# Kernel optimization log

Hardware: AMD Instinct MI355X
Metric: run time of the kernel (lower is better)

Reference implementation:

```python
import jax, jax.numpy as jnp
import numpy as np


def gcn_conv(x, edge_index, W, b):
    """PyG GCNConv with default add_self_loops=True, normalize=True.

    edge_index[0] = source (j), edge_index[1] = target (i), flow source_to_target.
    norm = deg^{-1/2}[j] * deg^{-1/2}[i], deg computed on target col with
    self-loops included (edge weight 1).
    """
    N = x.shape[0]
    loops = jnp.arange(N, dtype=edge_index.dtype)
    row = jnp.concatenate([edge_index[0], loops])  # sources j
    col = jnp.concatenate([edge_index[1], loops])  # targets i

    ones = jnp.ones(row.shape[0], dtype=x.dtype)
    deg = jax.ops.segment_sum(ones, col, num_segments=N)  # [N]
    deg_inv_sqrt = jnp.where(deg > 0, jax.lax.rsqrt(deg), 0.0)
    norm = deg_inv_sqrt[row] * deg_inv_sqrt[col]  # [E+N]

    h = x @ W  # [N, out] linear transform before propagation
    msg = norm[:, None] * h[row]  # gather from sources
    out = jax.ops.segment_sum(msg, col, num_segments=N)  # scatter-add to targets
    return out + b


def setup_inputs() -> dict:
    key = jax.random.key(0)
    k1, k2, k3, k4 = jax.random.split(key, 4)
    N, E = 100000, 1600000
    d_in, d_hid, d_out = 128, 128, 64
    x = jax.random.normal(k1, (N, d_in), dtype=jnp.float32)
    edge_index = jax.random.randint(k2, (2, E), 0, N, dtype=jnp.int32)
    # Glorot-ish init for weights
    W1 = jax.random.normal(k3, (d_in, d_hid), dtype=jnp.float32) / np.sqrt(d_in)
    b1 = jnp.zeros((d_hid,), dtype=jnp.float32)
    W2 = jax.random.normal(k4, (d_hid, d_out), dtype=jnp.float32) / np.sqrt(d_hid)
    b2 = jnp.zeros((d_out,), dtype=jnp.float32)
    return {"x": x, "edge_index": edge_index, "W1": W1, "b1": b1, "W2": W2, "b2": b2}


def reference(x, edge_index, W1, b1, W2, b2):
    h = gcn_conv(x, edge_index, W1, b1)
    h = jax.nn.relu(h)
    out = gcn_conv(h, edge_index, W2, b2)
    return out
```

## Files before the change

kernel.cpp:

```cpp
#include <hip/hip_runtime.h>

typedef unsigned int uint;
typedef unsigned short ushort;
typedef short s8v __attribute__((ext_vector_type(8)));
typedef float f4v __attribute__((ext_vector_type(4)));

#define BSHIFT 8
#define NBUCK_MAX 512
#define PART_CH 4096


__device__ __forceinline__ uint f2bf(float f) {
    uint b = __float_as_uint(f);
    return (b + 0x7fffu + ((b >> 16) & 1u)) >> 16;
}
__device__ __forceinline__ uint pack2(float a, float b) {
    return f2bf(a) | (f2bf(b) << 16);
}
__device__ __forceinline__ float bflo(uint u) { return __uint_as_float(u << 16); }
__device__ __forceinline__ float bfhi(uint u) { return __uint_as_float(u & 0xffff0000u); }


__global__ __launch_bounds__(256) void hist_k(const int* __restrict__ dst, int E, int nbuck,
                                              int* __restrict__ bcnt) {
    __shared__ int h[NBUCK_MAX];
    int t = threadIdx.x;
    for (int i = t; i < nbuck; i += 256) h[i] = 0;
    __syncthreads();
    int e0 = blockIdx.x * PART_CH;
    int e1 = min(e0 + PART_CH, E);
    for (int e = e0 + t; e < e1; e += 256) atomicAdd(&h[((uint)dst[e]) >> BSHIFT], 1);
    __syncthreads();
    for (int i = t; i < nbuck; i += 256) {
        int v = h[i];
        if (v) atomicAdd(&bcnt[i], v);
    }
}

__global__ __launch_bounds__(512) void bscan_k(const int* __restrict__ bcnt, int nbuck, int E,
                                               int* __restrict__ bo, int* __restrict__ bcur) {
    __shared__ int s[512];
    int t = threadIdx.x;
    int v = (t < nbuck) ? bcnt[t] : 0;
    s[t] = v;
    __syncthreads();
    for (int off = 1; off < 512; off <<= 1) {
        int x = (t >= off) ? s[t - off] : 0;
        __syncthreads();
        s[t] += x;
        __syncthreads();
    }
    int excl = s[t] - v;
    if (t < nbuck) { bo[t] = excl; bcur[t] = excl; }
    if (t == 0) bo[nbuck] = E;
}

__global__ __launch_bounds__(256) void part_k(const int* __restrict__ src,
                                              const int* __restrict__ dst, int E, int nbuck,
                                              int* __restrict__ bcur, uint* __restrict__ eb) {
    __shared__ int h[NBUCK_MAX];
    __shared__ int cur[NBUCK_MAX];
    int t = threadIdx.x;
    for (int i = t; i < nbuck; i += 256) h[i] = 0;
    __syncthreads();
    int e0 = blockIdx.x * PART_CH;
    int e1 = min(e0 + PART_CH, E);
    for (int e = e0 + t; e < e1; e += 256) atomicAdd(&h[((uint)dst[e]) >> BSHIFT], 1);
    __syncthreads();
    for (int i = t; i < nbuck; i += 256) {
        int v = h[i];
        cur[i] = v ? atomicAdd(&bcur[i], v) : 0;
    }
    __syncthreads();
    for (int e = e0 + t; e < e1; e += 256) {
        int d = dst[e];
        int b = ((uint)d) >> BSHIFT;
        int p = atomicAdd(&cur[b], 1);
        eb[p] = ((uint)src[e] << BSHIFT) | (uint)(d & 255);
    }
}

__global__ __launch_bounds__(256) void build_k(const uint* __restrict__ eb,
                                               const int* __restrict__ bo, int N, int E,
                                               int* __restrict__ rowptr,
                                               float* __restrict__ dinv,
                                               int* __restrict__ csr) {
    __shared__ int c[256];
    __shared__ int s[256];
    int b = blockIdx.x;
    int t = threadIdx.x;
    int node0 = b << BSHIFT;
    int beg = bo[b], end = bo[b + 1];
    c[t] = 0;
    __syncthreads();
    for (int e = beg + t; e < end; e += 256) atomicAdd(&c[eb[e] & 255], 1);
    __syncthreads();
    int v = c[t];
    s[t] = v;
    __syncthreads();
    for (int off = 1; off < 256; off <<= 1) {
        int x = (t >= off) ? s[t - off] : 0;
        __syncthreads();
        s[t] += x;
        __syncthreads();
    }
    int excl = s[t] - v;
    int node = node0 + t;
    if (node < N) {
        rowptr[node] = beg + excl;
        dinv[node] = rsqrtf((float)(1 + v));
    }
    if (b == 0 && t == 0) rowptr[N] = E;
    __syncthreads();
    c[t] = beg + excl;
    __syncthreads();
    for (int e = beg + t; e < end; e += 256) {
        uint pk = eb[e];
        int p = atomicAdd(&c[pk & 255], 1);
        csr[p] = (int)(pk >> BSHIFT);
    }
}


template <int OUTC>
__global__ void wtrans_k(const float* __restrict__ W, ushort* __restrict__ Wt) {
    int c = blockIdx.x * 64 + threadIdx.x;
    if (c >= OUTC) return;
    for (int k0 = 0; k0 < 128; k0 += 8) {
        float v[8];
#pragma unroll
        for (int i = 0; i < 8; ++i) v[i] = W[(size_t)(k0 + i) * OUTC + c];
        uint4 p;
        p.x = pack2(v[0], v[1]);
        p.y = pack2(v[2], v[3]);
        p.z = pack2(v[4], v[5]);
        p.w = pack2(v[6], v[7]);
        *(uint4*)(Wt + (size_t)c * 128 + k0) = p;
    }
}


template <int OUTC, bool AF32>
__global__ __launch_bounds__(256) void gemm_mfma(const void* __restrict__ Ain,
                                                 const ushort* __restrict__ Wt,
                                                 const float* __restrict__ dinv,
                                                 ushort* __restrict__ hs, int N) {
    constexpr int NT = OUTC / 16;
    constexpr int LDK = 136;
    __shared__ ushort Al[64 * LDK];
    __shared__ ushort Wl[OUTC * LDK];

    int tid = threadIdx.x;
    int row0 = blockIdx.x * 64;

    {
        int r = tid >> 2, seg = tid & 3;
        int gr = row0 + r;
        if (gr > N - 1) gr = N - 1;
        ushort* dstp = &Al[r * LDK + seg * 32];
        if (AF32) {
            const float4* ap = (const float4*)((const float*)Ain + (size_t)gr * 128 + seg * 32);
#pragma unroll
            for (int i = 0; i < 4; ++i) {
                float4 f0 = ap[2 * i], f1 = ap[2 * i + 1];
                uint4 u;
                u.x = pack2(f0.x, f0.y);
                u.y = pack2(f0.z, f0.w);
                u.z = pack2(f1.x, f1.y);
                u.w = pack2(f1.z, f1.w);
                *(uint4*)(dstp + i * 8) = u;
            }
        } else {
            const uint4* ap = (const uint4*)((const ushort*)Ain + (size_t)gr * 128 + seg * 32);
#pragma unroll
            for (int i = 0; i < 4; ++i) *(uint4*)(dstp + i * 8) = ap[i];
        }
    }
    {
        const uint4* wp = (const uint4*)Wt;
        for (int idx = tid; idx < OUTC * 16; idx += 256) {
            int r = idx >> 4, c = idx & 15;
            *(uint4*)(&Wl[r * LDK + c * 8]) = wp[idx];
        }
    }
    __syncthreads();

    int w = tid >> 6;
    int l = tid & 63;
    int lo = l & 15, q = l >> 4;

    f4v acc[NT];
#pragma unroll
    for (int i = 0; i < NT; ++i) acc[i] = (f4v){0.f, 0.f, 0.f, 0.f};

#pragma unroll
    for (int ks = 0; ks < 4; ++ks) {
        s8v af = *(const s8v*)&Al[(16 * w + lo) * LDK + ks * 32 + q * 8];
#pragma unroll
        for (int nt = 0; nt < NT; ++nt) {
            s8v wf = *(const s8v*)&Wl[(nt * 16 + lo) * LDK + ks * 32 + q * 8];
            acc[nt] = __builtin_amdgcn_mfma_f32_16x16x32_bf16(wf, af, acc[nt], 0, 0, 0);
        }
    }

    int grow = row0 + 16 * w + lo;
    if (grow < N) {
        float dr = dinv[grow];
        ushort* orow = hs + (size_t)grow * OUTC + q * 4;
#pragma unroll
        for (int nt = 0; nt < NT; ++nt) {
            uint2 p;
            p.x = pack2(acc[nt][0] * dr, acc[nt][1] * dr);
            p.y = pack2(acc[nt][2] * dr, acc[nt][3] * dr);
            *(uint2*)(orow + nt * 16) = p;
        }
    }
}


template <int C, bool RELU, bool OUTBF>
__global__ __launch_bounds__(256) void aggregate_k(const ushort* __restrict__ hs,
                                                   const float* __restrict__ dinv,
                                                   const int* __restrict__ rowptr,
                                                   const int* __restrict__ csr,
                                                   const float* __restrict__ bias,
                                                   void* __restrict__ out, int N) {
    constexpr int LANES = C / 8;
    constexpr int NPB = 256 / LANES;
    int tid = threadIdx.x;
    int sub = tid / LANES;
    int lane = tid % LANES;
    int node = blockIdx.x * NPB + sub;
    if (node >= N) return;

    const uint4* h4 = (const uint4*)hs;
    float accA[8], accB[8];
    {
        uint4 v = h4[(size_t)node * LANES + lane];
        accA[0] = bflo(v.x); accA[1] = bfhi(v.x);
        accA[2] = bflo(v.y); accA[3] = bfhi(v.y);
        accA[4] = bflo(v.z); accA[5] = bfhi(v.z);
        accA[6] = bflo(v.w); accA[7] = bfhi(v.w);
    }
#pragma unroll
    for (int k = 0; k < 8; ++k) accB[k] = 0.f;

    int beg = rowptr[node];
    int end = rowptr[node + 1];
    int e = beg;
    for (; e + 8 <= end; e += 8) {
        int j[8];
#pragma unroll
        for (int k = 0; k < 8; ++k) j[k] = csr[e + k];
        uint4 v[8];
#pragma unroll
        for (int k = 0; k < 8; ++k) v[k] = h4[(size_t)j[k] * LANES + lane];
#pragma unroll
        for (int k = 0; k < 8; ++k) {
            float* a = (k & 1) ? accB : accA;
            a[0] += bflo(v[k].x); a[1] += bfhi(v[k].x);
            a[2] += bflo(v[k].y); a[3] += bfhi(v[k].y);
            a[4] += bflo(v[k].z); a[5] += bfhi(v[k].z);
            a[6] += bflo(v[k].w); a[7] += bfhi(v[k].w);
        }
    }
    if (e + 4 <= end) {
        int j0 = csr[e + 0];
        int j1 = csr[e + 1];
        int j2 = csr[e + 2];
        int j3 = csr[e + 3];
        uint4 v0 = h4[(size_t)j0 * LANES + lane];
        uint4 v1 = h4[(size_t)j1 * LANES + lane];
        uint4 v2 = h4[(size_t)j2 * LANES + lane];
        uint4 v3 = h4[(size_t)j3 * LANES + lane];
        accA[0] += bflo(v0.x) + bflo(v2.x); accA[1] += bfhi(v0.x) + bfhi(v2.x);
        accA[2] += bflo(v0.y) + bflo(v2.y); accA[3] += bfhi(v0.y) + bfhi(v2.y);
        accA[4] += bflo(v0.z) + bflo(v2.z); accA[5] += bfhi(v0.z) + bfhi(v2.z);
        accA[6] += bflo(v0.w) + bflo(v2.w); accA[7] += bfhi(v0.w) + bfhi(v2.w);
        accB[0] += bflo(v1.x) + bflo(v3.x); accB[1] += bfhi(v1.x) + bfhi(v3.x);
        accB[2] += bflo(v1.y) + bflo(v3.y); accB[3] += bfhi(v1.y) + bfhi(v3.y);
        accB[4] += bflo(v1.z) + bflo(v3.z); accB[5] += bfhi(v1.z) + bfhi(v3.z);
        accB[6] += bflo(v1.w) + bflo(v3.w); accB[7] += bfhi(v1.w) + bfhi(v3.w);
        e += 4;
    }
    for (; e < end; ++e) {
        int j = csr[e];
        uint4 v = h4[(size_t)j * LANES + lane];
        accA[0] += bflo(v.x); accA[1] += bfhi(v.x);
        accA[2] += bflo(v.y); accA[3] += bfhi(v.y);
        accA[4] += bflo(v.z); accA[5] += bfhi(v.z);
        accA[6] += bflo(v.w); accA[7] += bfhi(v.w);
    }

    float di = dinv[node];
    const float4* b4 = (const float4*)(bias + lane * 8);
    float4 b0 = b4[0], b1 = b4[1];
    float o[8];
    o[0] = fmaf(di, accA[0] + accB[0], b0.x);
    o[1] = fmaf(di, accA[1] + accB[1], b0.y);
    o[2] = fmaf(di, accA[2] + accB[2], b0.z);
    o[3] = fmaf(di, accA[3] + accB[3], b0.w);
    o[4] = fmaf(di, accA[4] + accB[4], b1.x);
    o[5] = fmaf(di, accA[5] + accB[5], b1.y);
    o[6] = fmaf(di, accA[6] + accB[6], b1.z);
    o[7] = fmaf(di, accA[7] + accB[7], b1.w);
    if (RELU) {
#pragma unroll
        for (int k = 0; k < 8; ++k) o[k] = fmaxf(o[k], 0.f);
    }
    if (OUTBF) {
        uint4 p;
        p.x = pack2(o[0], o[1]);
        p.y = pack2(o[2], o[3]);
        p.z = pack2(o[4], o[5]);
        p.w = pack2(o[6], o[7]);
        ((uint4*)out)[(size_t)node * LANES + lane] = p;
    } else {
        float4* op = (float4*)((float*)out + (size_t)node * C + lane * 8);
        op[0] = make_float4(o[0], o[1], o[2], o[3]);
        op[1] = make_float4(o[4], o[5], o[6], o[7]);
    }
}


extern "C" void kernel_launch(void* const* d_in, const int* in_sizes, int n_in,
                              void* d_out, int out_size, void* d_ws, size_t ws_size,
                              hipStream_t stream) {
    const float* x  = (const float*)d_in[0];
    const int*   ei = (const int*)d_in[1];
    const float* W1 = (const float*)d_in[2];
    const float* b1 = (const float*)d_in[3];
    const float* W2 = (const float*)d_in[4];
    const float* b2 = (const float*)d_in[5];
    float* out = (float*)d_out;

    const int D = 128;
    int N = in_sizes[0] / D;
    int E = in_sizes[1] / 2;
    const int* src = ei;
    const int* dst = ei + E;

    int nbuck = (N + 255) >> BSHIFT;

    char* ws = (char*)d_ws;
    size_t off = 0;
    auto alloc = [&](size_t bytes) -> void* {
        void* p = ws + off;
        off += (bytes + 255) & ~(size_t)255;
        return p;
    };
    int*    bcnt  = (int*)alloc((size_t)NBUCK_MAX * 4);
    int*    bo    = (int*)alloc((size_t)(NBUCK_MAX + 1) * 4);
    int*    bcur  = (int*)alloc((size_t)NBUCK_MAX * 4);
    int*    rowptr= (int*)alloc((size_t)(N + 1) * 4);
    float*  dinv  = (float*)alloc((size_t)N * 4);
    uint*   eb    = (uint*)alloc((size_t)E * 4);
    int*    csr   = (int*)alloc((size_t)E * 4);
    ushort* wt1   = (ushort*)alloc((size_t)128 * 128 * 2);
    ushort* wt2   = (ushort*)alloc((size_t)64 * 128 * 2);
    ushort* hs1   = (ushort*)alloc((size_t)N * 128 * 2);
    ushort* h1a   = (ushort*)alloc((size_t)N * 128 * 2);
    ushort* hs2   = hs1;

    int PB = (E + PART_CH - 1) / PART_CH;

    hipMemsetAsync(bcnt, 0, (size_t)NBUCK_MAX * 4, stream);
    hist_k<<<PB, 256, 0, stream>>>(dst, E, nbuck, bcnt);
    bscan_k<<<1, 512, 0, stream>>>(bcnt, nbuck, E, bo, bcur);
    part_k<<<PB, 256, 0, stream>>>(src, dst, E, nbuck, bcur, eb);
    build_k<<<nbuck, 256, 0, stream>>>(eb, bo, N, E, rowptr, dinv, csr);
    wtrans_k<128><<<2, 64, 0, stream>>>(W1, wt1);
    wtrans_k<64><<<1, 64, 0, stream>>>(W2, wt2);

    int gG = (N + 63) / 64;
    gemm_mfma<128, true><<<gG, 256, 0, stream>>>(x, wt1, dinv, hs1, N);
    aggregate_k<128, true, true><<<(N + 15) / 16, 256, 0, stream>>>(hs1, dinv, rowptr, csr, b1, h1a, N);
    gemm_mfma<64, false><<<gG, 256, 0, stream>>>(h1a, wt2, dinv, hs2, N);
    aggregate_k<64, false, false><<<(N + 31) / 32, 256, 0, stream>>>(hs2, dinv, rowptr, csr, b2, out, N);
}
```

Measured before the change: 205.0 us.

## Store GEMM output in 16-column slices and aggregate per slice for cache locality

The GEMM now writes its bf16 output in a slice-major layout, with each 16-column slice stored contiguously across all nodes. Aggregation runs one block per (64-node chunk, slice) pair, with consecutive blocks covering different slices of the same nodes. Each slice's working set is N*32 bytes, small enough to stay resident in L2/LLC during the random neighbor gathers. The cost is re-reading the CSR indices and rowptr once per slice, plus smaller 8-byte gathers that may use memory transactions less efficiently. The partition chunk size is also doubled.

```diff
diff --git a/kernel.cpp b/kernel.cpp
--- a/kernel.cpp
+++ b/kernel.cpp
@@ -7,7 +7,7 @@
 
 #define BSHIFT 8
 #define NBUCK_MAX 512
-#define PART_CH 4096
+#define PART_CH 8192
 
 
 __device__ __forceinline__ uint f2bf(float f) {
@@ -206,44 +206,42 @@
     int grow = row0 + 16 * w + lo;
     if (grow < N) {
         float dr = dinv[grow];
-        ushort* orow = hs + (size_t)grow * OUTC + q * 4;
 #pragma unroll
         for (int nt = 0; nt < NT; ++nt) {
             uint2 p;
             p.x = pack2(acc[nt][0] * dr, acc[nt][1] * dr);
             p.y = pack2(acc[nt][2] * dr, acc[nt][3] * dr);
-            *(uint2*)(orow + nt * 16) = p;
-        }
-    }
-}
-
-
-template <int C, bool RELU, bool OUTBF>
-__global__ __launch_bounds__(256) void aggregate_k(const ushort* __restrict__ hs,
-                                                   const float* __restrict__ dinv,
-                                                   const int* __restrict__ rowptr,
-                                                   const int* __restrict__ csr,
-                                                   const float* __restrict__ bias,
-                                                   void* __restrict__ out, int N) {
-    constexpr int LANES = C / 8;
-    constexpr int NPB = 256 / LANES;
+            *(uint2*)(hs + ((size_t)nt * N + grow) * 16 + q * 4) = p;
+        }
+    }
+}
+
+
+template <int C, int NSL, bool RELU, bool OUTBF>
+__global__ __launch_bounds__(256) void aggregate_sl(const ushort* __restrict__ hs,
+                                                    const float* __restrict__ dinv,
+                                                    const int* __restrict__ rowptr,
+                                                    const int* __restrict__ csr,
+                                                    const float* __restrict__ bias,
+                                                    void* __restrict__ out, int N) {
+    int bid = blockIdx.x;
+    int slice = bid & (NSL - 1);
+    int chunk = bid / NSL;
     int tid = threadIdx.x;
-    int sub = tid / LANES;
-    int lane = tid % LANES;
-    int node = blockIdx.x * NPB + sub;
+    int g = tid >> 2;
+    int lane = tid & 3;
+    int node = chunk * 64 + g;
     if (node >= N) return;
 
-    const uint4* h4 = (const uint4*)hs;
-    float accA[8], accB[8];
+    const uint2* h2 = (const uint2*)(hs + (size_t)slice * N * 16);
+    float accA[4], accB[4];
     {
-        uint4 v = h4[(size_t)node * LANES + lane];
+        uint2 v = h2[(size_t)node * 4 + lane];
         accA[0] = bflo(v.x); accA[1] = bfhi(v.x);
         accA[2] = bflo(v.y); accA[3] = bfhi(v.y);
-        accA[4] = bflo(v.z); accA[5] = bfhi(v.z);
-        accA[6] = bflo(v.w); accA[7] = bfhi(v.w);
-    }
-#pragma unroll
-    for (int k = 0; k < 8; ++k) accB[k] = 0.f;
+    }
+#pragma unroll
+    for (int k = 0; k < 4; ++k) accB[k] = 0.f;
 
     int beg = rowptr[node];
     int end = rowptr[node + 1];
@@ -252,73 +250,53 @@
         int j[8];
 #pragma unroll
         for (int k = 0; k < 8; ++k) j[k] = csr[e + k];
-        uint4 v[8];
-#pragma unroll
-        for (int k = 0; k < 8; ++k) v[k] = h4[(size_t)j[k] * LANES + lane];
+        uint2 v[8];
+#pragma unroll
+        for (int k = 0; k < 8; ++k) v[k] = h2[(size_t)j[k] * 4 + lane];
 #pragma unroll
         for (int k = 0; k < 8; ++k) {
             float* a = (k & 1) ? accB : accA;
             a[0] += bflo(v[k].x); a[1] += bfhi(v[k].x);
             a[2] += bflo(v[k].y); a[3] += bfhi(v[k].y);
-            a[4] += bflo(v[k].z); a[5] += bfhi(v[k].z);
-            a[6] += bflo(v[k].w); a[7] += bfhi(v[k].w);
         }
     }
     if (e + 4 <= end) {
-        int j0 = csr[e + 0];
-        int j1 = csr[e + 1];
-        int j2 = csr[e + 2];
-        int j3 = csr[e + 3];
-        uint4 v0 = h4[(size_t)j0 * LANES + lane];
-        uint4 v1 = h4[(size_t)j1 * LANES + lane];
-        uint4 v2 = h4[(size_t)j2 * LANES + lane];
-        uint4 v3 = h4[(size_t)j3 * LANES + lane];
+        int j0 = csr[e], j1 = csr[e + 1], j2 = csr[e + 2], j3 = csr[e + 3];
+        uint2 v0 = h2[(size_t)j0 * 4 + lane];
+        uint2 v1 = h2[(size_t)j1 * 4 + lane];
+        uint2 v2 = h2[(size_t)j2 * 4 + lane];
+        uint2 v3 = h2[(size_t)j3 * 4 + lane];
         accA[0] += bflo(v0.x) + bflo(v2.x); accA[1] += bfhi(v0.x) + bfhi(v2.x);
         accA[2] += bflo(v0.y) + bflo(v2.y); accA[3] += bfhi(v0.y) + bfhi(v2.y);
-        accA[4] += bflo(v0.z) + bflo(v2.z); accA[5] += bfhi(v0.z) + bfhi(v2.z);
-        accA[6] += bflo(v0.w) + bflo(v2.w); accA[7] += bfhi(v0.w) + bfhi(v2.w);
         accB[0] += bflo(v1.x) + bflo(v3.x); accB[1] += bfhi(v1.x) + bfhi(v3.x);
         accB[2] += bflo(v1.y) + bflo(v3.y); accB[3] += bfhi(v1.y) + bfhi(v3.y);
-        accB[4] += bflo(v1.z) + bflo(v3.z); accB[5] += bfhi(v1.z) + bfhi(v3.z);
-        accB[6] += bflo(v1.w) + bflo(v3.w); accB[7] += bfhi(v1.w) + bfhi(v3.w);
         e += 4;
     }
     for (; e < end; ++e) {
-        int j = csr[e];
-        uint4 v = h4[(size_t)j * LANES + lane];
+        uint2 v = h2[(size_t)csr[e] * 4 + lane];
         accA[0] += bflo(v.x); accA[1] += bfhi(v.x);
         accA[2] += bflo(v.y); accA[3] += bfhi(v.y);
-        accA[4] += bflo(v.z); accA[5] += bfhi(v.z);
-        accA[6] += bflo(v.w); accA[7] += bfhi(v.w);
     }
 
     float di = dinv[node];
-    const float4* b4 = (const float4*)(bias + lane * 8);
-    float4 b0 = b4[0], b1 = b4[1];
-    float o[8];
-    o[0] = fmaf(di, accA[0] + accB[0], b0.x);
-    o[1] = fmaf(di, accA[1] + accB[1], b0.y);
-    o[2] = fmaf(di, accA[2] + accB[2], b0.z);
-    o[3] = fmaf(di, accA[3] + accB[3], b0.w);
-    o[4] = fmaf(di, accA[4] + accB[4], b1.x);
-    o[5] = fmaf(di, accA[5] + accB[5], b1.y);
-    o[6] = fmaf(di, accA[6] + accB[6], b1.z);
-    o[7] = fmaf(di, accA[7] + accB[7], b1.w);
+    float4 bv = *(const float4*)(bias + slice * 16 + lane * 4);
+    float o[4];
+    o[0] = fmaf(di, accA[0] + accB[0], bv.x);
+    o[1] = fmaf(di, accA[1] + accB[1], bv.y);
+    o[2] = fmaf(di, accA[2] + accB[2], bv.z);
+    o[3] = fmaf(di, accA[3] + accB[3], bv.w);
     if (RELU) {
 #pragma unroll
-        for (int k = 0; k < 8; ++k) o[k] = fmaxf(o[k], 0.f);
+        for (int k = 0; k < 4; ++k) o[k] = fmaxf(o[k], 0.f);
     }
     if (OUTBF) {
-        uint4 p;
+        uint2 p;
         p.x = pack2(o[0], o[1]);
         p.y = pack2(o[2], o[3]);
-        p.z = pack2(o[4], o[5]);
-        p.w = pack2(o[6], o[7]);
-        ((uint4*)out)[(size_t)node * LANES + lane] = p;
+        *(uint2*)((ushort*)out + (size_t)node * C + slice * 16 + lane * 4) = p;
     } else {
-        float4* op = (float4*)((float*)out + (size_t)node * C + lane * 8);
-        op[0] = make_float4(o[0], o[1], o[2], o[3]);
-        op[1] = make_float4(o[4], o[5], o[6], o[7]);
+        *(float4*)((float*)out + (size_t)node * C + slice * 16 + lane * 4) =
+            make_float4(o[0], o[1], o[2], o[3]);
     }
 }
 
@@ -373,8 +351,9 @@
     wtrans_k<64><<<1, 64, 0, stream>>>(W2, wt2);
 
     int gG = (N + 63) / 64;
+    int chunks = (N + 63) / 64;
     gemm_mfma<128, true><<<gG, 256, 0, stream>>>(x, wt1, dinv, hs1, N);
-    aggregate_k<128, true, true><<<(N + 15) / 16, 256, 0, stream>>>(hs1, dinv, rowptr, csr, b1, h1a, N);
+    aggregate_sl<128, 8, true, true><<<chunks * 8, 256, 0, stream>>>(hs1, dinv, rowptr, csr, b1, h1a, N);
     gemm_mfma<64, false><<<gG, 256, 0, stream>>>(h1a, wt2, dinv, hs2, N);
-    aggregate_k<64, false, false><<<(N + 31) / 32, 256, 0, stream>>>(hs2, dinv, rowptr, csr, b2, out, N);
-}
+    aggregate_sl<64, 4, false, false><<<chunks * 4, 256, 0, stream>>>(hs2, dinv, rowptr, csr, b2, out, N);
+}
```

Result: slower. 243.4 us (+18.7%).

## Slice features into 16-column planes and degree-sort nodes for aggregation

Applied to the files above, without the earlier changes.

The GEMM output is now stored as feature-sliced planes of 16 bf16 columns per node. Each aggregation block handles one slice for 128 nodes, so the gather working set per slice fits better in cache. Nodes are reordered by degree through a histogram, scan and placement pass, which balances the work inside each wavefront. The cost is several extra small kernels, CSR indices being re-read once per slice, and 32-byte gathers per node that may use memory transactions less efficiently. PART_CH is also doubled.

```diff
diff --git a/kernel.cpp b/kernel.cpp
--- a/kernel.cpp
+++ b/kernel.cpp
@@ -7,7 +7,8 @@
 
 #define BSHIFT 8
 #define NBUCK_MAX 512
-#define PART_CH 4096
+#define PART_CH 8192
+#define DBINS 128
 
 
 __device__ __forceinline__ uint f2bf(float f) {
@@ -83,7 +84,6 @@
 __global__ __launch_bounds__(256) void build_k(const uint* __restrict__ eb,
                                                const int* __restrict__ bo, int N, int E,
                                                int* __restrict__ rowptr,
-                                               float* __restrict__ dinv,
                                                int* __restrict__ csr) {
     __shared__ int c[256];
     __shared__ int s[256];
@@ -106,10 +106,7 @@
     }
     int excl = s[t] - v;
     int node = node0 + t;
-    if (node < N) {
-        rowptr[node] = beg + excl;
-        dinv[node] = rsqrtf((float)(1 + v));
-    }
+    if (node < N) rowptr[node] = beg + excl;
     if (b == 0 && t == 0) rowptr[N] = E;
     __syncthreads();
     c[t] = beg + excl;
@@ -119,6 +116,60 @@
         int p = atomicAdd(&c[pk & 255], 1);
         csr[p] = (int)(pk >> BSHIFT);
     }
+}
+
+
+__global__ void dinv_k(const int* __restrict__ rowptr, float* __restrict__ dinv, int N) {
+    int i = blockIdx.x * blockDim.x + threadIdx.x;
+    if (i < N) dinv[i] = rsqrtf((float)(1 + rowptr[i + 1] - rowptr[i]));
+}
+
+
+__global__ __launch_bounds__(256) void dhist_k(const int* __restrict__ rowptr, int N,
+                                               int* __restrict__ dh) {
+    __shared__ int h[DBINS];
+    int t = threadIdx.x;
+    if (t < DBINS) h[t] = 0;
+    __syncthreads();
+    int i = blockIdx.x * 256 + t;
+    if (i < N) {
+        int deg = rowptr[i + 1] - rowptr[i];
+        atomicAdd(&h[min(deg, DBINS - 1)], 1);
+    }
+    __syncthreads();
+    if (t < DBINS) {
+        int v = h[t];
+        if (v) atomicAdd(&dh[t], v);
+    }
+}
+
+__global__ void dscan_k(const int* __restrict__ dh, int* __restrict__ dcur) {
+    __shared__ int s[DBINS];
+    int t = threadIdx.x;
+    int v = dh[t];
+    s[t] = v;
+    __syncthreads();
+    for (int off = 1; off < DBINS; off <<= 1) {
+        int x = (t >= off) ? s[t - off] : 0;
+        __syncthreads();
+        s[t] += x;
+        __syncthreads();
+    }
+    dcur[t] = s[t] - v;
+}
+
+__global__ __launch_bounds__(256) void dplace_k(const int* __restrict__ rowptr, int N,
+                                                int* __restrict__ dcur,
+                                                int* __restrict__ perm,
+                                                int2* __restrict__ rp2) {
+    int i = blockIdx.x * 256 + threadIdx.x;
+    if (i >= N) return;
+    int beg = rowptr[i];
+    int end = rowptr[i + 1];
+    int bin = min(end - beg, DBINS - 1);
+    int pos = atomicAdd(&dcur[bin], 1);
+    perm[pos] = i;
+    rp2[pos] = make_int2(beg, end);
 }
 
 
@@ -206,37 +257,40 @@
     int grow = row0 + 16 * w + lo;
     if (grow < N) {
         float dr = dinv[grow];
-        ushort* orow = hs + (size_t)grow * OUTC + q * 4;
 #pragma unroll
         for (int nt = 0; nt < NT; ++nt) {
             uint2 p;
             p.x = pack2(acc[nt][0] * dr, acc[nt][1] * dr);
             p.y = pack2(acc[nt][2] * dr, acc[nt][3] * dr);
-            *(uint2*)(orow + nt * 16) = p;
+            *(uint2*)(hs + ((size_t)nt * N + grow) * 16 + q * 4) = p;
         }
     }
 }
 
 
-template <int C, bool RELU, bool OUTBF>
-__global__ __launch_bounds__(256) void aggregate_k(const ushort* __restrict__ hs,
-                                                   const float* __restrict__ dinv,
-                                                   const int* __restrict__ rowptr,
-                                                   const int* __restrict__ csr,
-                                                   const float* __restrict__ bias,
-                                                   void* __restrict__ out, int N) {
-    constexpr int LANES = C / 8;
-    constexpr int NPB = 256 / LANES;
+template <int C, int NSL, bool RELU, bool OUTBF>
+__global__ __launch_bounds__(256) void aggregate_sl2(const ushort* __restrict__ hs,
+                                                     const int* __restrict__ perm,
+                                                     const int2* __restrict__ rp2,
+                                                     const int* __restrict__ csr,
+                                                     const float* __restrict__ bias,
+                                                     void* __restrict__ out, int N) {
+    int bid = blockIdx.x;
+    int slice = bid & (NSL - 1);
+    int chunk = bid / NSL;
     int tid = threadIdx.x;
-    int sub = tid / LANES;
-    int lane = tid % LANES;
-    int node = blockIdx.x * NPB + sub;
-    if (node >= N) return;
-
-    const uint4* h4 = (const uint4*)hs;
+    int pair = tid >> 1;
+    int half = tid & 1;
+    int pos = chunk * 128 + pair;
+    if (pos >= N) return;
+    int node = perm[pos];
+    int2 rp = rp2[pos];
+    float di = rsqrtf((float)(1 + rp.y - rp.x));
+
+    const uint4* h4 = (const uint4*)(hs + (size_t)slice * N * 16);
     float accA[8], accB[8];
     {
-        uint4 v = h4[(size_t)node * LANES + lane];
+        uint4 v = h4[(size_t)node * 2 + half];
         accA[0] = bflo(v.x); accA[1] = bfhi(v.x);
         accA[2] = bflo(v.y); accA[3] = bfhi(v.y);
         accA[4] = bflo(v.z); accA[5] = bfhi(v.z);
@@ -245,16 +299,14 @@
 #pragma unroll
     for (int k = 0; k < 8; ++k) accB[k] = 0.f;
 
-    int beg = rowptr[node];
-    int end = rowptr[node + 1];
-    int e = beg;
+    int e = rp.x, end = rp.y;
     for (; e + 8 <= end; e += 8) {
         int j[8];
 #pragma unroll
         for (int k = 0; k < 8; ++k) j[k] = csr[e + k];
         uint4 v[8];
 #pragma unroll
-        for (int k = 0; k < 8; ++k) v[k] = h4[(size_t)j[k] * LANES + lane];
+        for (int k = 0; k < 8; ++k) v[k] = h4[(size_t)j[k] * 2 + half];
 #pragma unroll
         for (int k = 0; k < 8; ++k) {
             float* a = (k & 1) ? accB : accA;
@@ -265,14 +317,11 @@
         }
     }
     if (e + 4 <= end) {
-        int j0 = csr[e + 0];
-        int j1 = csr[e + 1];
-        int j2 = csr[e + 2];
-        int j3 = csr[e + 3];
-        uint4 v0 = h4[(size_t)j0 * LANES + lane];
-        uint4 v1 = h4[(size_t)j1 * LANES + lane];
-        uint4 v2 = h4[(size_t)j2 * LANES + lane];
-        uint4 v3 = h4[(size_t)j3 * LANES + lane];
+        int j0 = csr[e], j1 = csr[e + 1], j2 = csr[e + 2], j3 = csr[e + 3];
+        uint4 v0 = h4[(size_t)j0 * 2 + half];
+        uint4 v1 = h4[(size_t)j1 * 2 + half];
+        uint4 v2 = h4[(size_t)j2 * 2 + half];
+        uint4 v3 = h4[(size_t)j3 * 2 + half];
         accA[0] += bflo(v0.x) + bflo(v2.x); accA[1] += bfhi(v0.x) + bfhi(v2.x);
         accA[2] += bflo(v0.y) + bflo(v2.y); accA[3] += bfhi(v0.y) + bfhi(v2.y);
         accA[4] += bflo(v0.z) + bflo(v2.z); accA[5] += bfhi(v0.z) + bfhi(v2.z);
@@ -284,16 +333,14 @@
         e += 4;
     }
     for (; e < end; ++e) {
-        int j = csr[e];
-        uint4 v = h4[(size_t)j * LANES + lane];
+        uint4 v = h4[(size_t)csr[e] * 2 + half];
         accA[0] += bflo(v.x); accA[1] += bfhi(v.x);
         accA[2] += bflo(v.y); accA[3] += bfhi(v.y);
         accA[4] += bflo(v.z); accA[5] += bfhi(v.z);
         accA[6] += bflo(v.w); accA[7] += bfhi(v.w);
     }
 
-    float di = dinv[node];
-    const float4* b4 = (const float4*)(bias + lane * 8);
+    const float4* b4 = (const float4*)(bias + slice * 16 + half * 8);
     float4 b0 = b4[0], b1 = b4[1];
     float o[8];
     o[0] = fmaf(di, accA[0] + accB[0], b0.x);
@@ -314,11 +361,11 @@
         p.y = pack2(o[2], o[3]);
         p.z = pack2(o[4], o[5]);
         p.w = pack2(o[6], o[7]);
-        ((uint4*)out)[(size_t)node * LANES + lane] = p;
+        *(uint4*)((ushort*)out + (size_t)node * C + slice * 16 + half * 8) = p;
     } else {
-        float4* op = (float4*)((float*)out + (size_t)node * C + lane * 8);
-        op[0] = make_float4(o[0], o[1], o[2], o[3]);
-        op[1] = make_float4(o[4], o[5], o[6], o[7]);
+        float* op = (float*)out + (size_t)node * C + slice * 16 + half * 8;
+        *(float4*)op = make_float4(o[0], o[1], o[2], o[3]);
+        *(float4*)(op + 4) = make_float4(o[4], o[5], o[6], o[7]);
     }
 }
 
@@ -352,8 +399,12 @@
     int*    bcnt  = (int*)alloc((size_t)NBUCK_MAX * 4);
     int*    bo    = (int*)alloc((size_t)(NBUCK_MAX + 1) * 4);
     int*    bcur  = (int*)alloc((size_t)NBUCK_MAX * 4);
+    int*    dh    = (int*)alloc((size_t)DBINS * 4);
+    int*    dcur  = (int*)alloc((size_t)DBINS * 4);
     int*    rowptr= (int*)alloc((size_t)(N + 1) * 4);
     float*  dinv  = (float*)alloc((size_t)N * 4);
+    int*    perm  = (int*)alloc((size_t)N * 4);
+    int2*   rp2   = (int2*)alloc((size_t)N * 8);
     uint*   eb    = (uint*)alloc((size_t)E * 4);
     int*    csr   = (int*)alloc((size_t)E * 4);
     ushort* wt1   = (ushort*)alloc((size_t)128 * 128 * 2);
@@ -363,18 +414,25 @@
     ushort* hs2   = hs1;
 
     int PB = (E + PART_CH - 1) / PART_CH;
+    int gN = (N + 255) / 256;
 
     hipMemsetAsync(bcnt, 0, (size_t)NBUCK_MAX * 4, stream);
+    hipMemsetAsync(dh, 0, (size_t)DBINS * 4, stream);
     hist_k<<<PB, 256, 0, stream>>>(dst, E, nbuck, bcnt);
     bscan_k<<<1, 512, 0, stream>>>(bcnt, nbuck, E, bo, bcur);
     part_k<<<PB, 256, 0, stream>>>(src, dst, E, nbuck, bcur, eb);
-    build_k<<<nbuck, 256, 0, stream>>>(eb, bo, N, E, rowptr, dinv, csr);
+    build_k<<<nbuck, 256, 0, stream>>>(eb, bo, N, E, rowptr, csr);
+    dinv_k<<<gN, 256, 0, stream>>>(rowptr, dinv, N);
+    dhist_k<<<gN, 256, 0, stream>>>(rowptr, N, dh);
+    dscan_k<<<1, DBINS, 0, stream>>>(dh, dcur);
+    dplace_k<<<gN, 256, 0, stream>>>(rowptr, N, dcur, perm, rp2);
     wtrans_k<128><<<2, 64, 0, stream>>>(W1, wt1);
     wtrans_k<64><<<1, 64, 0, stream>>>(W2, wt2);
 
     int gG = (N + 63) / 64;
+    int chunks = (N + 127) / 128;
     gemm_mfma<128, true><<<gG, 256, 0, stream>>>(x, wt1, dinv, hs1, N);
-    aggregate_k<128, true, true><<<(N + 15) / 16, 256, 0, stream>>>(hs1, dinv, rowptr, csr, b1, h1a, N);
+    aggregate_sl2<128, 8, true, true><<<chunks * 8, 256, 0, stream>>>(hs1, perm, rp2, csr, b1, h1a, N);
     gemm_mfma<64, false><<<gG, 256, 0, stream>>>(h1a, wt2, dinv, hs2, N);
-    aggregate_k<64, false, false><<<(N + 31) / 32, 256, 0, stream>>>(hs2, dinv, rowptr, csr, b2, out, N);
-}
+    aggregate_sl2<64, 4, false, false><<<chunks * 4, 256, 0, stream>>>(hs2, perm, rp2, csr, b2, out, N);
+}
```

New measurement: 552.9 us. 2.7x slower.
